# Kernel optimization log

Measured on AMD Instinct MI355X. Metric: run time of the kernel, lower is better.

Reference implementation:

```python
import jax, jax.numpy as jnp
import numpy as np

B, N, H = 4096, 64, 16  # batch, board side, max hints per row/col
FALLBACK_SIZE = 12


def setup_inputs() -> dict:
    key = jax.random.key(0)
    k1, k2, k3, k4 = jax.random.split(key, 4)
    grid = jax.random.normal(k1, (B, 1, N, N), dtype=jnp.float32)
    hints = jax.random.randint(k2, (B, 2, N, H), 0, 3).astype(jnp.float32)
    w_g = jax.random.normal(k3, (1, N, N), dtype=jnp.float32)
    w_h = jax.random.normal(k4, (2, N, H), dtype=jnp.float32)
    return {"grid": grid, "hints": hints, "w_g": w_g, "w_h": w_h}


def reference(grid, hints, w_g, w_h):
    # neural energy: simple linear energy head standing in for self.model(grid, hints)
    neural_energy = jnp.mean(
        jnp.einsum('bchw,chw->b', grid, w_g)
        + jnp.einsum('bkhm,khm->b', hints, w_h)
    )

    n = grid.shape[2]
    sg = jax.nn.sigmoid(grid[:, 0] * 3.0)          # [B,N,N] soft grid
    row_hints = hints[:, 0]                         # [B,N,H]
    col_hints = hints[:, 1]                         # [B,N,H]

    # per-sample puzzle size: last row/col index that has any hint, +1; else 12
    idx = jnp.arange(n)
    row_has = row_hints.sum(-1) > 0                 # [B,N]
    col_has = col_hints.sum(-1) > 0                 # [B,N]
    last_r = jnp.max(jnp.where(row_has, idx, -1), axis=1)
    last_c = jnp.max(jnp.where(col_has, idx, -1), axis=1)
    size = jnp.where((last_r >= 0) & (last_c >= 0),
                     jnp.maximum(last_r, last_c) + 1,
                     FALLBACK_SIZE)                 # [B]
    m = (idx[None, :] < size[:, None]).astype(grid.dtype)  # [B,N] validity mask
    sz = size.astype(grid.dtype)

    # logic energy: masked row/col sum MSE (sum reduction / size), mean over batch * 10
    row_target = row_hints.sum(-1)                  # [B,N]
    col_target = col_hints.sum(-1)                  # [B,N]
    actual_rows = jnp.einsum('bij,bj->bi', sg, m)   # sum over cols j < size
    actual_cols = jnp.einsum('bij,bi->bj', sg, m)   # sum over rows i < size
    row_err = jnp.sum((actual_rows - row_target) ** 2 * m, axis=-1) / sz
    col_err = jnp.sum((actual_cols - col_target) ** 2 * m, axis=-1) / sz
    logic_energy = jnp.mean(row_err + col_err) * 10.0

    # binary energy: mean of grid^2 over the size x size sub-board, mean over batch * 0.1
    m2 = m[:, :, None] * m[:, None, :]              # [B,N,N]
    bin_per = jnp.sum(grid[:, 0] ** 2 * m2, axis=(1, 2)) / (sz * sz)
    binary_energy = jnp.mean(bin_per) * 0.1

    return neural_energy + logic_energy + binary_energy
```

## Files before the change

kernel.cpp:

```cpp
#include <hip/hip_runtime.h>

#define B_TOT 4096

__global__ __launch_bounds__(256) void energy_kernel(
    const float* __restrict__ grid,
    const float* __restrict__ hints,
    const float* __restrict__ w_g,
    const float* __restrict__ w_h,
    float* __restrict__ ws)
{
    const int b    = blockIdx.x;
    const int tid  = threadIdx.x;
    const int lane = tid & 63;
    const int wv   = tid >> 6;

    __shared__ float  target[2][64];
    __shared__ float4 colp4[4][16];
    __shared__ float  red[4];

    const float* hb = hints + (size_t)b * 2048;
    const float* gb = grid  + (size_t)b * 4096;

    float4 h0 = *(const float4*)(hb + 8 * tid);
    float4 h1 = *(const float4*)(hb + 8 * tid + 4);
    float4 g0 = *(const float4*)(gb + 4 * tid);
    float4 g1 = *(const float4*)(gb + 4 * tid + 1024);
    float4 g2 = *(const float4*)(gb + 4 * tid + 2048);
    float4 g3 = *(const float4*)(gb + 4 * tid + 3072);
    float4 wh0 = *(const float4*)(w_h + 8 * tid);
    float4 wh1 = *(const float4*)(w_h + 8 * tid + 4);
    float4 wg0 = *(const float4*)(w_g + 4 * tid);
    float4 wg1 = *(const float4*)(w_g + 4 * tid + 1024);
    float4 wg2 = *(const float4*)(w_g + 4 * tid + 2048);
    float4 wg3 = *(const float4*)(w_g + 4 * tid + 3072);

    float neural = h0.x * wh0.x + h0.y * wh0.y + h0.z * wh0.z + h0.w * wh0.w
                 + h1.x * wh1.x + h1.y * wh1.y + h1.z * wh1.z + h1.w * wh1.w;
    float hsum = h0.x + h0.y + h0.z + h0.w + h1.x + h1.y + h1.z + h1.w;
    hsum += __shfl_xor(hsum, 1);
    if ((tid & 1) == 0) target[tid >> 7][(tid >> 1) & 63] = hsum;
    __syncthreads();

    unsigned long long mr = __ballot(target[0][lane] > 0.f);
    unsigned long long mc = __ballot(target[1][lane] > 0.f);
    int lr = mr ? (63 - __builtin_clzll(mr)) : -1;
    int lc = mc ? (63 - __builtin_clzll(mc)) : -1;
    const int   size = (lr >= 0 && lc >= 0) ? (max(lr, lc) + 1) : 12;
    const float sz   = (float)size;

    const int c0    = (tid & 15) * 4;
    const int rbase = tid >> 4;
    const float mx = (c0 + 0 < size) ? 1.f : 0.f;
    const float my = (c0 + 1 < size) ? 1.f : 0.f;
    const float mz = (c0 + 2 < size) ? 1.f : 0.f;
    const float mw = (c0 + 3 < size) ? 1.f : 0.f;

    float binp = 0.f, errp = 0.f;
    float4 cacc = {0.f, 0.f, 0.f, 0.f};
    float4 gk[4] = {g0, g1, g2, g3};
    float4 wk[4] = {wg0, wg1, wg2, wg3};

    #pragma unroll
    for (int k = 0; k < 4; ++k) {
        float4 g = gk[k];
        float4 w = wk[k];
        neural += g.x * w.x + g.y * w.y + g.z * w.z + g.w * w.w;
        int   row   = rbase + 16 * k;
        float rmask = (row < size) ? 1.f : 0.f;
        binp += rmask * (mx * g.x * g.x + my * g.y * g.y + mz * g.z * g.z + mw * g.w * g.w);

        float sx  = __builtin_amdgcn_rcpf(1.f + __expf(-3.f * g.x));
        float sy  = __builtin_amdgcn_rcpf(1.f + __expf(-3.f * g.y));
        float sz_ = __builtin_amdgcn_rcpf(1.f + __expf(-3.f * g.z));
        float sw  = __builtin_amdgcn_rcpf(1.f + __expf(-3.f * g.w));

        float rs = mx * sx + my * sy + mz * sz_ + mw * sw;
        rs += __shfl_xor(rs, 1);
        rs += __shfl_xor(rs, 2);
        rs += __shfl_xor(rs, 4);
        rs += __shfl_xor(rs, 8);
        if ((lane & 15) == 0 && row < size) {
            float d = rs - target[0][row];
            errp += d * d;
        }

        cacc.x += rmask * sx;
        cacc.y += rmask * sy;
        cacc.z += rmask * sz_;
        cacc.w += rmask * sw;
    }

    cacc.x += __shfl_xor(cacc.x, 16); cacc.x += __shfl_xor(cacc.x, 32);
    cacc.y += __shfl_xor(cacc.y, 16); cacc.y += __shfl_xor(cacc.y, 32);
    cacc.z += __shfl_xor(cacc.z, 16); cacc.z += __shfl_xor(cacc.z, 32);
    cacc.w += __shfl_xor(cacc.w, 16); cacc.w += __shfl_xor(cacc.w, 32);
    if (lane < 16) colp4[wv][lane] = cacc;
    __syncthreads();

    if (tid < 64) {
        const float* cp = (const float*)colp4;
        float csum = cp[tid] + cp[64 + tid] + cp[128 + tid] + cp[192 + tid];
        if (tid < size) {
            float d = csum - target[1][tid];
            errp += d * d;
        }
    }

    float v = neural + errp * (10.f / sz) + binp * (0.1f / (sz * sz));
    #pragma unroll
    for (int off = 1; off < 64; off <<= 1) v += __shfl_xor(v, off);
    if (lane == 0) red[wv] = v;
    __syncthreads();
    if (tid == 0) ws[b] = red[0] + red[1] + red[2] + red[3];
}

__global__ __launch_bounds__(1024) void final_reduce_kernel(
    const float* __restrict__ ws, float* __restrict__ out)
{
    const int tid = threadIdx.x;
    float4 v4 = ((const float4*)ws)[tid];
    float v = v4.x + v4.y + v4.z + v4.w;
    #pragma unroll
    for (int off = 1; off < 64; off <<= 1) v += __shfl_xor(v, off);
    __shared__ float r[16];
    if ((tid & 63) == 0) r[tid >> 6] = v;
    __syncthreads();
    if (tid < 16) {
        float t = r[tid];
        t += __shfl_xor(t, 1);
        t += __shfl_xor(t, 2);
        t += __shfl_xor(t, 4);
        t += __shfl_xor(t, 8);
        if (tid == 0) out[0] = t * (1.f / (float)B_TOT);
    }
}

extern "C" void kernel_launch(void* const* d_in, const int* in_sizes, int n_in,
                              void* d_out, int out_size, void* d_ws, size_t ws_size,
                              hipStream_t stream) {
    const float* grid_p  = (const float*)d_in[0];
    const float* hints_p = (const float*)d_in[1];
    const float* w_g     = (const float*)d_in[2];
    const float* w_h     = (const float*)d_in[3];
    float* out = (float*)d_out;
    float* ws  = (float*)d_ws;

    energy_kernel<<<B_TOT, 256, 0, stream>>>(grid_p, hints_p, w_g, w_h, ws);
    final_reduce_kernel<<<1, 1024, 0, stream>>>(ws, out);
}
```

Measured before the change: 120.6 us.

## Map one wavefront per sample and drop block-level synchronization

Each 64-lane wavefront now handles a whole sample, with four samples per 256-thread block, in place of one block per sample. Row and column targets, the size detection and the column sums are done inside the wave using shuffles and per-wave shared memory, which removes all __syncthreads and the cross-wave reduction. Each lane now streams 16 grid float4s and 8 hint float4s in loops, so the grid has a quarter as many blocks. The cost is less memory-level parallelism per thread, since loads are issued in an unroll-4 loop instead of all up front.

```diff
diff --git a/kernel.cpp b/kernel.cpp
--- a/kernel.cpp
+++ b/kernel.cpp
@@ -9,84 +9,75 @@
     const float* __restrict__ w_h,
     float* __restrict__ ws)
 {
-    const int b    = blockIdx.x;
     const int tid  = threadIdx.x;
     const int lane = tid & 63;
     const int wv   = tid >> 6;
+    const int b    = (blockIdx.x << 2) + wv;
 
-    __shared__ float  target[2][64];
-    __shared__ float4 colp4[4][16];
-    __shared__ float  red[4];
+    __shared__ __align__(16) float tgt[4][2][64];
 
     const float* hb = hints + (size_t)b * 2048;
     const float* gb = grid  + (size_t)b * 4096;
 
-    float4 h0 = *(const float4*)(hb + 8 * tid);
-    float4 h1 = *(const float4*)(hb + 8 * tid + 4);
-    float4 g0 = *(const float4*)(gb + 4 * tid);
-    float4 g1 = *(const float4*)(gb + 4 * tid + 1024);
-    float4 g2 = *(const float4*)(gb + 4 * tid + 2048);
-    float4 g3 = *(const float4*)(gb + 4 * tid + 3072);
-    float4 wh0 = *(const float4*)(w_h + 8 * tid);
-    float4 wh1 = *(const float4*)(w_h + 8 * tid + 4);
-    float4 wg0 = *(const float4*)(w_g + 4 * tid);
-    float4 wg1 = *(const float4*)(w_g + 4 * tid + 1024);
-    float4 wg2 = *(const float4*)(w_g + 4 * tid + 2048);
-    float4 wg3 = *(const float4*)(w_g + 4 * tid + 3072);
+    float neural = 0.f;
 
-    float neural = h0.x * wh0.x + h0.y * wh0.y + h0.z * wh0.z + h0.w * wh0.w
-                 + h1.x * wh1.x + h1.y * wh1.y + h1.z * wh1.z + h1.w * wh1.w;
-    float hsum = h0.x + h0.y + h0.z + h0.w + h1.x + h1.y + h1.z + h1.w;
-    hsum += __shfl_xor(hsum, 1);
-    if ((tid & 1) == 0) target[tid >> 7][(tid >> 1) & 63] = hsum;
-    __syncthreads();
+    #pragma unroll
+    for (int j = 0; j < 8; ++j) {
+        float4 h  = *(const float4*)(hb  + 256 * j + 4 * lane);
+        float4 wh = *(const float4*)(w_h + 256 * j + 4 * lane);
+        neural += h.x * wh.x + h.y * wh.y + h.z * wh.z + h.w * wh.w;
+        float s = h.x + h.y + h.z + h.w;
+        s += __shfl_xor(s, 1);
+        s += __shfl_xor(s, 2);
+        if ((lane & 3) == 0) {
+            int r = 16 * j + (lane >> 2);
+            tgt[wv][r >> 6][r & 63] = s;
+        }
+    }
 
-    unsigned long long mr = __ballot(target[0][lane] > 0.f);
-    unsigned long long mc = __ballot(target[1][lane] > 0.f);
+    unsigned long long mr = __ballot(tgt[wv][0][lane] > 0.f);
+    unsigned long long mc = __ballot(tgt[wv][1][lane] > 0.f);
     int lr = mr ? (63 - __builtin_clzll(mr)) : -1;
     int lc = mc ? (63 - __builtin_clzll(mc)) : -1;
     const int   size = (lr >= 0 && lc >= 0) ? (max(lr, lc) + 1) : 12;
     const float sz   = (float)size;
 
-    const int c0    = (tid & 15) * 4;
-    const int rbase = tid >> 4;
+    const int c0 = (lane & 15) << 2;
     const float mx = (c0 + 0 < size) ? 1.f : 0.f;
     const float my = (c0 + 1 < size) ? 1.f : 0.f;
     const float mz = (c0 + 2 < size) ? 1.f : 0.f;
     const float mw = (c0 + 3 < size) ? 1.f : 0.f;
+    const float lm0 = ((lane & 15) == 0) ? 1.f : 0.f;
 
     float binp = 0.f, errp = 0.f;
     float4 cacc = {0.f, 0.f, 0.f, 0.f};
-    float4 gk[4] = {g0, g1, g2, g3};
-    float4 wk[4] = {wg0, wg1, wg2, wg3};
 
-    #pragma unroll
-    for (int k = 0; k < 4; ++k) {
-        float4 g = gk[k];
-        float4 w = wk[k];
+    #pragma unroll 4
+    for (int j = 0; j < 16; ++j) {
+        float4 g = *(const float4*)(gb  + 256 * j + 4 * lane);
+        float4 w = *(const float4*)(w_g + 256 * j + 4 * lane);
         neural += g.x * w.x + g.y * w.y + g.z * w.z + g.w * w.w;
-        int   row   = rbase + 16 * k;
-        float rmask = (row < size) ? 1.f : 0.f;
+
+        const int   row   = 4 * j + (lane >> 4);
+        const float rmask = (row < size) ? 1.f : 0.f;
         binp += rmask * (mx * g.x * g.x + my * g.y * g.y + mz * g.z * g.z + mw * g.w * g.w);
 
-        float sx  = __builtin_amdgcn_rcpf(1.f + __expf(-3.f * g.x));
-        float sy  = __builtin_amdgcn_rcpf(1.f + __expf(-3.f * g.y));
-        float sz_ = __builtin_amdgcn_rcpf(1.f + __expf(-3.f * g.z));
-        float sw  = __builtin_amdgcn_rcpf(1.f + __expf(-3.f * g.w));
+        float sx = __builtin_amdgcn_rcpf(1.f + __expf(-3.f * g.x));
+        float sy = __builtin_amdgcn_rcpf(1.f + __expf(-3.f * g.y));
+        float s2 = __builtin_amdgcn_rcpf(1.f + __expf(-3.f * g.z));
+        float sw = __builtin_amdgcn_rcpf(1.f + __expf(-3.f * g.w));
 
-        float rs = mx * sx + my * sy + mz * sz_ + mw * sw;
+        float rs = mx * sx + my * sy + mz * s2 + mw * sw;
         rs += __shfl_xor(rs, 1);
         rs += __shfl_xor(rs, 2);
         rs += __shfl_xor(rs, 4);
         rs += __shfl_xor(rs, 8);
-        if ((lane & 15) == 0 && row < size) {
-            float d = rs - target[0][row];
-            errp += d * d;
-        }
+        float d = rs - tgt[wv][0][row];
+        errp += lm0 * rmask * d * d;
 
         cacc.x += rmask * sx;
         cacc.y += rmask * sy;
-        cacc.z += rmask * sz_;
+        cacc.z += rmask * s2;
         cacc.w += rmask * sw;
     }
 
@@ -94,24 +85,17 @@
     cacc.y += __shfl_xor(cacc.y, 16); cacc.y += __shfl_xor(cacc.y, 32);
     cacc.z += __shfl_xor(cacc.z, 16); cacc.z += __shfl_xor(cacc.z, 32);
     cacc.w += __shfl_xor(cacc.w, 16); cacc.w += __shfl_xor(cacc.w, 32);
-    if (lane < 16) colp4[wv][lane] = cacc;
-    __syncthreads();
 
-    if (tid < 64) {
-        const float* cp = (const float*)colp4;
-        float csum = cp[tid] + cp[64 + tid] + cp[128 + tid] + cp[192 + tid];
-        if (tid < size) {
-            float d = csum - target[1][tid];
-            errp += d * d;
-        }
+    if (lane < 16) {
+        float4 t = *(const float4*)&tgt[wv][1][c0];
+        float dx = cacc.x - t.x, dy = cacc.y - t.y, dz = cacc.z - t.z, dw = cacc.w - t.w;
+        errp += mx * dx * dx + my * dy * dy + mz * dz * dz + mw * dw * dw;
     }
 
     float v = neural + errp * (10.f / sz) + binp * (0.1f / (sz * sz));
     #pragma unroll
     for (int off = 1; off < 64; off <<= 1) v += __shfl_xor(v, off);
-    if (lane == 0) red[wv] = v;
-    __syncthreads();
-    if (tid == 0) ws[b] = red[0] + red[1] + red[2] + red[3];
+    if (lane == 0) ws[b] = v;
 }
 
 __global__ __launch_bounds__(1024) void final_reduce_kernel(
@@ -145,6 +129,6 @@
     float* out = (float*)d_out;
     float* ws  = (float*)d_ws;
 
-    energy_kernel<<<B_TOT, 256, 0, stream>>>(grid_p, hints_p, w_g, w_h, ws);
+    energy_kernel<<<B_TOT / 4, 256, 0, stream>>>(grid_p, hints_p, w_g, w_h, ws);
     final_reduce_kernel<<<1, 1024, 0, stream>>>(ws, out);
 }
```

After: 122.1 us. Within noise of the previous version (+1.3%).
